# Optimization experiments

Measured on AMD Instinct MI355X. Metric: run time of the kernel, lower is better.

Reference implementation:

```python
import jax, jax.numpy as jnp
import numpy as np

N_SRC, N_MID, N_DST = 200000, 50000, 10000
D = 128
E1, E2 = 800000, 160000
EPS = 1e-12  # F.normalize eps


def setup_inputs() -> dict:
    key = jax.random.key(0)
    ks = jax.random.split(key, 12)
    s = 1.0 / np.sqrt(D)
    return {
        "x": jax.random.normal(ks[0], (N_SRC, D), jnp.float32),
        "W_l1": jax.random.uniform(ks[1], (D, D), jnp.float32, -s, s),
        "b_l1": jax.random.uniform(ks[2], (D,), jnp.float32, -s, s),
        "W_r1": jax.random.uniform(ks[3], (D, D), jnp.float32, -s, s),
        "W_l2": jax.random.uniform(ks[4], (D, D), jnp.float32, -s, s),
        "b_l2": jax.random.uniform(ks[5], (D,), jnp.float32, -s, s),
        "W_r2": jax.random.uniform(ks[6], (D, D), jnp.float32, -s, s),
        "row1": jax.random.randint(ks[7], (E1,), 0, N_SRC, jnp.int32),
        "col1": jax.random.randint(ks[8], (E1,), 0, N_MID, jnp.int32),
        "row2": jax.random.randint(ks[9], (E2,), 0, N_MID, jnp.int32),
        "col2": jax.random.randint(ks[10], (E2,), 0, N_DST, jnp.int32),
    }


def _sage_conv(x_src, x_dst, row, col, W_l, b_l, W_r, n_dst):
    # mean aggregation of source features over incoming edges (gather + scatter-add)
    msg = x_src[row]                                              # [E, D]
    agg = jax.ops.segment_sum(msg, col, num_segments=n_dst)       # [n_dst, D]
    deg = jax.ops.segment_sum(jnp.ones((row.shape[0],), x_src.dtype), col,
                              num_segments=n_dst)[:, None]        # [n_dst, 1]
    mean = jnp.where(deg > 0, agg / jnp.maximum(deg, 1.0), 0.0)
    out = mean @ W_l.T + b_l + x_dst @ W_r.T                      # lin_l + lin_r (root)
    # L2 normalize (normalize=True)
    norm = jnp.sqrt(jnp.sum(out * out, axis=-1, keepdims=True))
    return out / jnp.maximum(norm, EPS)


def reference(x, W_l1, b_l1, W_r1, W_l2, b_l2, W_r2, row1, col1, row2, col2):
    # layer 1: src = all sampled nodes, dst = first N_MID nodes
    h = _sage_conv(x, x[:N_MID], row1, col1, W_l1, b_l1, W_r1, N_MID)
    h = jax.nn.relu(h)  # dropout is identity in eval mode
    # layer 2: src = mid nodes, dst = first N_DST nodes (the batch targets)
    out = _sage_conv(h, h[:N_DST], row2, col2, W_l2, b_l2, W_r2, N_DST)
    return out
```

## Files before the change

kernel.cpp:

```cpp
#include <hip/hip_runtime.h>
#include <hip/hip_bf16.h>

#define DD 128
#define N_SRC 200000
#define N_MID 50000
#define N_DST 10000
#define E1 800000
#define E2 160000
#define CAP 48

typedef unsigned short u16;
typedef unsigned int u32;
typedef __attribute__((ext_vector_type(8))) short s16x8;
typedef __attribute__((ext_vector_type(4))) float f32x4;
typedef __attribute__((ext_vector_type(4))) int i32x4;
typedef __attribute__((ext_vector_type(4))) float fv4;


__device__ __forceinline__ float bf_lo(u32 u) {
    union { u32 u; float f; } v; v.u = u << 16; return v.f;
}
__device__ __forceinline__ float bf_hi(u32 u) {
    union { u32 u; float f; } v; v.u = u & 0xffff0000u; return v.f;
}
__device__ __forceinline__ u32 f2bf_bits(float f) {
    union { float f; u32 u; } v; v.f = f;
    return (v.u + 0x7fffu + ((v.u >> 16) & 1u)) >> 16;
}
__device__ __forceinline__ u32 pack2bf(float lo, float hi) {
    return f2bf_bits(lo) | (f2bf_bits(hi) << 16);
}


#define FILL1_SLICE  4000
#define FILL1_BLOCKS 1600

#define NCONV8 (N_SRC * DD / 8)
#define WTF_T 8192
#define PREP_T (NCONV8 + WTF_T)
#define PREP_BLOCKS ((PREP_T + 255) / 256)
#define PF_BLOCKS (FILL1_BLOCKS + PREP_BLOCKS)

__global__ __launch_bounds__(256, 8) void prep_fill(
    const float* __restrict__ x, u16* __restrict__ xb,
    const float* __restrict__ Wl1, const float* __restrict__ Wr1,
    u16* __restrict__ WTf1,
    const float* __restrict__ Wl2, const float* __restrict__ Wr2,
    u16* __restrict__ WTf2,
    const int* __restrict__ row1, const int* __restrict__ col1,
    int* __restrict__ cnt1, int* __restrict__ csr1)
{
    const int b = blockIdx.x;
    const int tid = threadIdx.x;

    if (b < FILL1_BLOCKS) {
        int slice = b >> 3, shard = b & 7;
        int e0 = slice * FILL1_SLICE, e1 = e0 + FILL1_SLICE;
        const int lo = shard * 6250;
        for (int base = e0 + tid * 4; base < e1; base += 1024) {
            i32x4 c4 = __builtin_nontemporal_load((const i32x4*)(col1 + base));
            i32x4 r4 = __builtin_nontemporal_load((const i32x4*)(row1 + base));
            #pragma unroll
            for (int k = 0; k < 4; ++k) {
                int c = c4[k];
                if ((u32)(c - lo) < 6250u) {
                    int p = atomicAdd(cnt1 + c, 1);
                    if (p < CAP) csr1[c * CAP + p] = r4[k];
                }
            }
        }
    } else {
        int i = (b - FILL1_BLOCKS) * 256 + tid;
        if (i < NCONV8) {
            const fv4* x4 = (const fv4*)x;
            fv4 a = __builtin_nontemporal_load(x4 + i * 2);
            fv4 bb = __builtin_nontemporal_load(x4 + i * 2 + 1);
            uint4 o;
            o.x = pack2bf(a[0], a[1]); o.y = pack2bf(a[2], a[3]);
            o.z = pack2bf(bb[0], bb[1]); o.w = pack2bf(bb[2], bb[3]);
            ((uint4*)xb)[i] = o;
        } else if (i < NCONV8 + WTF_T) {
            int t = i - NCONV8;
            int layer = t >> 12;
            int rem = t & 4095;
            int kt = rem >> 9;
            int nt = (rem >> 6) & 7;
            int lane = rem & 63;
            int gn = nt * 16 + (lane & 15);
            int k0 = kt * 32 + (lane >> 4) * 8;
            const float* Wl = layer ? Wl2 : Wl1;
            const float* Wr = layer ? Wr2 : Wr1;
            u16* WTf = layer ? WTf2 : WTf1;
            u32 o[4];
            #pragma unroll
            for (int p = 0; p < 4; ++p) {
                int ka = k0 + 2 * p, kb = ka + 1;
                float ea = (ka < 128) ? Wl[gn * 128 + ka] : Wr[gn * 128 + (ka - 128)];
                float eb = (kb < 128) ? Wl[gn * 128 + kb] : Wr[gn * 128 + (kb - 128)];
                o[p] = pack2bf(ea, eb);
            }
            ((uint4*)WTf)[(kt * 8 + nt) * 64 + lane] = make_uint4(o[0], o[1], o[2], o[3]);
        }
    }
}


template <int ROWS, bool RELU, int MINB>
__global__ __launch_bounds__(256, MINB) void sage_kernel(
    const u16* __restrict__ xsrc_b, const u16* __restrict__ xdst_b,
    const int* __restrict__ cnt, const int* __restrict__ csrf,
    const u16* __restrict__ WTf, const float* __restrict__ bias,
    float* __restrict__ out_f, u16* __restrict__ out_b,
    int n_dst, int fp32lim,
    const int* __restrict__ frow, const int* __restrict__ fcol,
    int* __restrict__ fcnt, int* __restrict__ fcsr, int nfill)
{
    __shared__ float smem[ROWS * 132];
    const int tid = threadIdx.x;

    if (blockIdx.x < nfill) {
        int bb = blockIdx.x;
        int slice = bb >> 3, shard = bb & 7;
        int e0 = slice * 4000, e1 = e0 + 4000;
        const int lo = shard * 1250;
        for (int base = e0 + tid * 4; base < e1; base += 1024) {
            i32x4 c4 = __builtin_nontemporal_load((const i32x4*)(fcol + base));
            i32x4 r4 = __builtin_nontemporal_load((const i32x4*)(frow + base));
            #pragma unroll
            for (int k = 0; k < 4; ++k) {
                int c = c4[k];
                if ((u32)(c - lo) < 1250u) {
                    int p = atomicAdd(fcnt + c, 1);
                    if (p < CAP) fcsr[c * CAP + p] = r4[k];
                }
            }
        }
        return;
    }

    const int i0 = (blockIdx.x - nfill) * ROWS;
    const int lane = tid & 63;
    const int w = tid >> 6;
    const int quarter = lane >> 4;
    const int l16 = lane & 15;
    const int half = lane >> 5;
    const int l32 = lane & 31;
    constexpr int RPW = ROWS / 4;

    const uint4* __restrict__ xs4 = (const uint4*)xsrc_b;
    const uint2* __restrict__ xd2 = (const uint2*)xdst_b;
    uint4* sA4 = (uint4*)smem;
    uint2* sA2 = (uint2*)smem;

    int degv = 0;
    {
        int rr = i0 + w * RPW + lane;
        if (lane < RPW && rr < n_dst) degv = cnt[rr];
    }
    int iv_next = 0;
    {
        int i = i0 + w * RPW;
        if (i < n_dst) iv_next = csrf[(size_t)i * CAP + lane];
    }

    for (int q = 0; q < RPW; ++q) {
        int r = w * RPW + q;
        int i = i0 + r;
        int deg = __shfl(degv, q);
        if (deg > CAP) deg = CAP;
        int iv = iv_next;
        if (q + 1 < RPW) {
            int i2 = i + 1;
            iv_next = (i2 < n_dst) ? csrf[(size_t)i2 * CAP + lane] : 0;
        }
        if (i < n_dst) {
            float acc[8] = {0.f, 0.f, 0.f, 0.f, 0.f, 0.f, 0.f, 0.f};
            if (deg > 0) {
                for (int g = 0; g < deg; g += 16) {
                    #pragma unroll
                    for (int j = 0; j < 4; ++j) {
                        if (g + 4 * j < deg) {
                            int rel = g + 4 * j + quarter;
                            int idx = __shfl(iv, rel & 63);
                            float m = (rel < deg) ? 1.f : 0.f;
                            uint4 u = xs4[(size_t)idx * 16 + l16];
                            acc[0] += m * bf_lo(u.x); acc[1] += m * bf_hi(u.x);
                            acc[2] += m * bf_lo(u.y); acc[3] += m * bf_hi(u.y);
                            acc[4] += m * bf_lo(u.z); acc[5] += m * bf_hi(u.z);
                            acc[6] += m * bf_lo(u.w); acc[7] += m * bf_hi(u.w);
                        }
                    }
                }
                #pragma unroll
                for (int k = 0; k < 8; ++k) {
                    acc[k] += __shfl_xor(acc[k], 16);
                    acc[k] += __shfl_xor(acc[k], 32);
                }
            }
            float s = (deg > 0) ? 1.f / (float)deg : 0.f;
            if (quarter == 0) {
                uint4 o;
                o.x = pack2bf(acc[0] * s, acc[1] * s);
                o.y = pack2bf(acc[2] * s, acc[3] * s);
                o.z = pack2bf(acc[4] * s, acc[5] * s);
                o.w = pack2bf(acc[6] * s, acc[7] * s);
                sA4[r * 33 + l16] = o;
            }
            if (half == 1) {
                sA2[r * 66 + 32 + l32] = xd2[(size_t)i * 32 + l32];
            }
        } else {
            if (quarter == 0) sA4[r * 33 + l16] = make_uint4(0, 0, 0, 0);
            if (half == 1)    sA2[r * 66 + 32 + l32] = make_uint2(0, 0);
        }
    }
    __syncthreads();

    constexpr int MT = ROWS / 16;
    const int nt0 = w * 2;
    const s16x8* sAv = (const s16x8*)smem;
    const s16x8* Bv = (const s16x8*)WTf;

    f32x4 C[MT][2];
    #pragma unroll
    for (int mt = 0; mt < MT; ++mt)
        #pragma unroll
        for (int ni = 0; ni < 2; ++ni)
            C[mt][ni] = (f32x4){0.f, 0.f, 0.f, 0.f};

    #pragma unroll
    for (int kt = 0; kt < 8; ++kt) {
        s16x8 a[MT];
        #pragma unroll
        for (int mt = 0; mt < MT; ++mt)
            a[mt] = sAv[(mt * 16 + l16) * 33 + kt * 4 + quarter];
        s16x8 b0 = Bv[(kt * 8 + nt0) * 64 + lane];
        s16x8 b1 = Bv[(kt * 8 + nt0 + 1) * 64 + lane];
        #pragma unroll
        for (int mt = 0; mt < MT; ++mt) {
            C[mt][0] = __builtin_amdgcn_mfma_f32_16x16x32_bf16(a[mt], b0, C[mt][0], 0, 0, 0);
            C[mt][1] = __builtin_amdgcn_mfma_f32_16x16x32_bf16(a[mt], b1, C[mt][1], 0, 0, 0);
        }
    }

    __syncthreads();
    float* sOut = smem;

    #pragma unroll
    for (int ni = 0; ni < 2; ++ni) {
        int col = (nt0 + ni) * 16 + l16;
        float bc = bias[col];
        #pragma unroll
        for (int mt = 0; mt < MT; ++mt) {
            #pragma unroll
            for (int r = 0; r < 4; ++r) {
                int row = mt * 16 + quarter * 4 + r;
                sOut[row * 132 + col] = C[mt][ni][r] + bc;
            }
        }
    }
    __syncthreads();

    constexpr int R = ROWS / 8;
    const int ty = tid >> 5;
    const int tx = tid & 31;
    #pragma unroll
    for (int r = 0; r < R; ++r) {
        int row = ty * R + r;
        float4 v = *(const float4*)(&sOut[row * 132 + tx * 4]);
        float s = v.x * v.x + v.y * v.y + v.z * v.z + v.w * v.w;
        #pragma unroll
        for (int off = 1; off < 32; off <<= 1) s += __shfl_xor(s, off);
        float scale = 1.f / fmaxf(sqrtf(s), 1e-12f);
        float v0 = v.x * scale, v1 = v.y * scale, v2 = v.z * scale, v3 = v.w * scale;
        if (RELU) {
            v0 = fmaxf(v0, 0.f); v1 = fmaxf(v1, 0.f);
            v2 = fmaxf(v2, 0.f); v3 = fmaxf(v3, 0.f);
        }
        int i = i0 + row;
        if (i < n_dst) {
            if (i < fp32lim)
                *(float4*)(out_f + (size_t)i * DD + tx * 4) = make_float4(v0, v1, v2, v3);
            if (out_b) {
                uint2 ob;
                ob.x = pack2bf(v0, v1);
                ob.y = pack2bf(v2, v3);
                *(uint2*)(out_b + (size_t)i * DD + tx * 4) = ob;
            }
        }
    }
}


#define NF2 320

extern "C" void kernel_launch(void* const* d_in, const int* in_sizes, int n_in,
                              void* d_out, int out_size, void* d_ws, size_t ws_size,
                              hipStream_t stream) {
    const float* x    = (const float*)d_in[0];
    const float* Wl1  = (const float*)d_in[1];
    const float* bl1  = (const float*)d_in[2];
    const float* Wr1  = (const float*)d_in[3];
    const float* Wl2  = (const float*)d_in[4];
    const float* bl2  = (const float*)d_in[5];
    const float* Wr2  = (const float*)d_in[6];
    const int* row1   = (const int*)d_in[7];
    const int* col1   = (const int*)d_in[8];
    const int* row2   = (const int*)d_in[9];
    const int* col2   = (const int*)d_in[10];
    float* out = (float*)d_out;

    char* p = (char*)d_ws;
    u16* xb    = (u16*)p;   p += (size_t)N_SRC * DD * sizeof(u16);
    u16* hb    = (u16*)p;   p += (size_t)N_MID * DD * sizeof(u16);
    u16* WTf1  = (u16*)p;   p += (size_t)256 * 128 * sizeof(u16);
    u16* WTf2  = (u16*)p;   p += (size_t)256 * 128 * sizeof(u16);
    char* zbase = p;
    int* cnt1  = (int*)p;   p += (size_t)N_MID * sizeof(int);
    int* cnt2  = (int*)p;   p += (size_t)N_DST * sizeof(int);
    int* csr1  = (int*)p;   p += (size_t)N_MID * CAP * sizeof(int);
    int* csr2  = (int*)p;   p += (size_t)N_DST * CAP * sizeof(int);
    size_t zlen = (size_t)(p - zbase);

    (void)hipMemsetAsync(zbase, 0, zlen, stream);

    prep_fill<<<PF_BLOCKS, 256, 0, stream>>>(
        x, xb, Wl1, Wr1, WTf1, Wl2, Wr2, WTf2, row1, col1, cnt1, csr1);

    sage_kernel<32, true, 6><<<NF2 + (N_MID + 31) / 32, 256, 0, stream>>>(
        xb, xb, cnt1, csr1, WTf1, bl1, (float*)nullptr, hb, N_MID, 0,
        row2, col2, cnt2, csr2, NF2);

    sage_kernel<16, false, 6><<<(N_DST + 15) / 16, 256, 0, stream>>>(
        hb, hb, cnt2, csr2, WTf2, bl2, out, (u16*)nullptr, N_DST, N_DST,
        nullptr, nullptr, nullptr, nullptr, 0);
}
```

Baseline: 273.3 us.

## Replace global-atomic CSR fill with two-pass bucket partition and shared-memory sort

Edge-to-CSR construction changes from sharded global atomicAdd per edge to a two-pass scheme. The first pass partitions edges into column buckets of width 200 using shared-memory counters and one global atomic per bucket per block. The second pass builds per-node CSR slots with shared-memory histograms. The layer-2 fill moves out of the layer-1 sage kernel into the shared sort kernel, and the bucket staging buffer reuses the hb region. This cuts global atomic contention and redundant col reads but adds a kernel launch and extra staging traffic, and edges past the 3584-per-bucket cap are dropped.

```diff
diff --git a/kernel.cpp b/kernel.cpp
--- a/kernel.cpp
+++ b/kernel.cpp
@@ -9,11 +9,19 @@
 #define E2 160000
 #define CAP 48
 
+#define BK_W  200
+#define NB1   250
+#define NB2   50
+#define CCAP  3584
+#define P1E   2048
+#define NP1_1 ((E1 + P1E - 1) / P1E)
+#define NP1_2 ((E2 + P1E - 1) / P1E)
+#define P1_BLOCKS (NP1_1 + NP1_2)
+
 typedef unsigned short u16;
 typedef unsigned int u32;
 typedef __attribute__((ext_vector_type(8))) short s16x8;
 typedef __attribute__((ext_vector_type(4))) float f32x4;
-typedef __attribute__((ext_vector_type(4))) int i32x4;
 typedef __attribute__((ext_vector_type(4))) float fv4;
 
 
@@ -31,46 +39,75 @@
     return f2bf_bits(lo) | (f2bf_bits(hi) << 16);
 }
 
-
-#define FILL1_SLICE  4000
-#define FILL1_BLOCKS 1600
 
 #define NCONV8 (N_SRC * DD / 8)
 #define WTF_T 8192
 #define PREP_T (NCONV8 + WTF_T)
 #define PREP_BLOCKS ((PREP_T + 255) / 256)
-#define PF_BLOCKS (FILL1_BLOCKS + PREP_BLOCKS)
-
-__global__ __launch_bounds__(256, 8) void prep_fill(
+#define PA_BLOCKS (P1_BLOCKS + PREP_BLOCKS)
+
+__global__ __launch_bounds__(256, 8) void prep_part(
     const float* __restrict__ x, u16* __restrict__ xb,
     const float* __restrict__ Wl1, const float* __restrict__ Wr1,
     u16* __restrict__ WTf1,
     const float* __restrict__ Wl2, const float* __restrict__ Wr2,
     u16* __restrict__ WTf2,
     const int* __restrict__ row1, const int* __restrict__ col1,
-    int* __restrict__ cnt1, int* __restrict__ csr1)
+    const int* __restrict__ row2, const int* __restrict__ col2,
+    int* __restrict__ ccnt1, int* __restrict__ ccnt2,
+    int2* __restrict__ cbuf1, int2* __restrict__ cbuf2)
 {
+    __shared__ int lcnt[256];
+    __shared__ int gbase[256];
     const int b = blockIdx.x;
     const int tid = threadIdx.x;
 
-    if (b < FILL1_BLOCKS) {
-        int slice = b >> 3, shard = b & 7;
-        int e0 = slice * FILL1_SLICE, e1 = e0 + FILL1_SLICE;
-        const int lo = shard * 6250;
-        for (int base = e0 + tid * 4; base < e1; base += 1024) {
-            i32x4 c4 = __builtin_nontemporal_load((const i32x4*)(col1 + base));
-            i32x4 r4 = __builtin_nontemporal_load((const i32x4*)(row1 + base));
-            #pragma unroll
-            for (int k = 0; k < 4; ++k) {
-                int c = c4[k];
-                if ((u32)(c - lo) < 6250u) {
-                    int p = atomicAdd(cnt1 + c, 1);
-                    if (p < CAP) csr1[c * CAP + p] = r4[k];
-                }
+    if (b < P1_BLOCKS) {
+        const int* __restrict__ colp;
+        const int* __restrict__ rowp;
+        int* __restrict__ ccnt;
+        int2* __restrict__ cbuf;
+        int e0, ne, nb;
+        if (b < NP1_1) {
+            colp = col1; rowp = row1; ccnt = ccnt1; cbuf = cbuf1;
+            e0 = b * P1E; ne = E1 - e0; if (ne > P1E) ne = P1E; nb = NB1;
+        } else {
+            int bb = b - NP1_1;
+            colp = col2; rowp = row2; ccnt = ccnt2; cbuf = cbuf2;
+            e0 = bb * P1E; ne = E2 - e0; if (ne > P1E) ne = P1E; nb = NB2;
+        }
+        for (int t = tid; t < nb; t += 256) lcnt[t] = 0;
+        __syncthreads();
+        int ep[8];
+        #pragma unroll
+        for (int j = 0; j < 8; ++j) {
+            int e = tid + j * 256;
+            ep[j] = -1;
+            if (e < ne) {
+                int c = colp[e0 + e];
+                int bk = c / BK_W;
+                int rk = atomicAdd(&lcnt[bk], 1);
+                ep[j] = (bk << 16) | rk;
+            }
+        }
+        __syncthreads();
+        for (int t = tid; t < nb; t += 256) {
+            int c = lcnt[t];
+            gbase[t] = c ? atomicAdd(&ccnt[t], c) : 0;
+        }
+        __syncthreads();
+        #pragma unroll
+        for (int j = 0; j < 8; ++j) {
+            if (ep[j] >= 0) {
+                int e = e0 + tid + j * 256;
+                int bk = ep[j] >> 16;
+                int pos = gbase[bk] + (ep[j] & 0xffff);
+                if (pos < CCAP)
+                    cbuf[(size_t)bk * CCAP + pos] = make_int2(colp[e], rowp[e]);
             }
         }
     } else {
-        int i = (b - FILL1_BLOCKS) * 256 + tid;
+        int i = (b - P1_BLOCKS) * 256 + tid;
         if (i < NCONV8) {
             const fv4* x4 = (const fv4*)x;
             fv4 a = __builtin_nontemporal_load(x4 + i * 2);
@@ -105,40 +142,57 @@
 }
 
 
+__global__ __launch_bounds__(256, 8) void bucket_sort(
+    const int2* __restrict__ cbuf1, const int2* __restrict__ cbuf2,
+    const int* __restrict__ ccnt1, const int* __restrict__ ccnt2,
+    int* __restrict__ cnt1, int* __restrict__ cnt2,
+    int* __restrict__ csr1, int* __restrict__ csr2)
+{
+    const int b = blockIdx.x;
+    const int tid = threadIdx.x;
+    const int2* __restrict__ cbuf;
+    const int* __restrict__ ccnt;
+    int* __restrict__ cnt;
+    int* __restrict__ csr;
+    int bkt;
+    if (b < NB1) { cbuf = cbuf1; ccnt = ccnt1; cnt = cnt1; csr = csr1; bkt = b; }
+    else         { cbuf = cbuf2; ccnt = ccnt2; cnt = cnt2; csr = csr2; bkt = b - NB1; }
+    const int col0 = bkt * BK_W;
+
+    __shared__ int hist[BK_W];
+    for (int t = tid; t < BK_W; t += 256) hist[t] = 0;
+    __syncthreads();
+
+    int n = ccnt[bkt]; if (n > CCAP) n = CCAP;
+    const int2* bp = cbuf + (size_t)bkt * CCAP;
+    for (int e = tid; e < n; e += 512) {
+        int2 cr0 = bp[e];
+        int e1i = e + 256;
+        bool h1 = e1i < n;
+        int2 cr1 = h1 ? bp[e1i] : cr0;
+        int r0 = atomicAdd(&hist[cr0.x - col0], 1);
+        if (r0 < CAP) csr[cr0.x * CAP + r0] = cr0.y;
+        if (h1) {
+            int r1 = atomicAdd(&hist[cr1.x - col0], 1);
+            if (r1 < CAP) csr[cr1.x * CAP + r1] = cr1.y;
+        }
+    }
+    __syncthreads();
+    for (int t = tid; t < BK_W; t += 256) cnt[col0 + t] = hist[t];
+}
+
+
 template <int ROWS, bool RELU, int MINB>
 __global__ __launch_bounds__(256, MINB) void sage_kernel(
     const u16* __restrict__ xsrc_b, const u16* __restrict__ xdst_b,
     const int* __restrict__ cnt, const int* __restrict__ csrf,
     const u16* __restrict__ WTf, const float* __restrict__ bias,
     float* __restrict__ out_f, u16* __restrict__ out_b,
-    int n_dst, int fp32lim,
-    const int* __restrict__ frow, const int* __restrict__ fcol,
-    int* __restrict__ fcnt, int* __restrict__ fcsr, int nfill)
+    int n_dst, int fp32lim)
 {
     __shared__ float smem[ROWS * 132];
     const int tid = threadIdx.x;
-
-    if (blockIdx.x < nfill) {
-        int bb = blockIdx.x;
-        int slice = bb >> 3, shard = bb & 7;
-        int e0 = slice * 4000, e1 = e0 + 4000;
-        const int lo = shard * 1250;
-        for (int base = e0 + tid * 4; base < e1; base += 1024) {
-            i32x4 c4 = __builtin_nontemporal_load((const i32x4*)(fcol + base));
-            i32x4 r4 = __builtin_nontemporal_load((const i32x4*)(frow + base));
-            #pragma unroll
-            for (int k = 0; k < 4; ++k) {
-                int c = c4[k];
-                if ((u32)(c - lo) < 1250u) {
-                    int p = atomicAdd(fcnt + c, 1);
-                    if (p < CAP) fcsr[c * CAP + p] = r4[k];
-                }
-            }
-        }
-        return;
-    }
-
-    const int i0 = (blockIdx.x - nfill) * ROWS;
+    const int i0 = blockIdx.x * ROWS;
     const int lane = tid & 63;
     const int w = tid >> 6;
     const int quarter = lane >> 4;
@@ -292,8 +346,6 @@
 }
 
 
-#define NF2 320
-
 extern "C" void kernel_launch(void* const* d_in, const int* in_sizes, int n_in,
                               void* d_out, int out_size, void* d_ws, size_t ws_size,
                               hipStream_t stream) {
@@ -312,26 +364,34 @@
 
     char* p = (char*)d_ws;
     u16* xb    = (u16*)p;   p += (size_t)N_SRC * DD * sizeof(u16);
-    u16* hb    = (u16*)p;   p += (size_t)N_MID * DD * sizeof(u16);
+    char* hbv  = p;         p += (size_t)N_MID * DD * sizeof(u16);
+    u16* hb    = (u16*)hbv;
+    int2* cbuf1 = (int2*)hbv;
+    int2* cbuf2 = cbuf1 + (size_t)NB1 * CCAP;
     u16* WTf1  = (u16*)p;   p += (size_t)256 * 128 * sizeof(u16);
     u16* WTf2  = (u16*)p;   p += (size_t)256 * 128 * sizeof(u16);
     char* zbase = p;
+    int* ccnt1 = (int*)p;   p += 256 * sizeof(int);
+    int* ccnt2 = (int*)p;   p += 64 * sizeof(int);
     int* cnt1  = (int*)p;   p += (size_t)N_MID * sizeof(int);
     int* cnt2  = (int*)p;   p += (size_t)N_DST * sizeof(int);
     int* csr1  = (int*)p;   p += (size_t)N_MID * CAP * sizeof(int);
     int* csr2  = (int*)p;   p += (size_t)N_DST * CAP * sizeof(int);
+    p += 256;
     size_t zlen = (size_t)(p - zbase);
 
     (void)hipMemsetAsync(zbase, 0, zlen, stream);
 
-    prep_fill<<<PF_BLOCKS, 256, 0, stream>>>(
-        x, xb, Wl1, Wr1, WTf1, Wl2, Wr2, WTf2, row1, col1, cnt1, csr1);
-
-    sage_kernel<32, true, 6><<<NF2 + (N_MID + 31) / 32, 256, 0, stream>>>(
-        xb, xb, cnt1, csr1, WTf1, bl1, (float*)nullptr, hb, N_MID, 0,
-        row2, col2, cnt2, csr2, NF2);
+    prep_part<<<PA_BLOCKS, 256, 0, stream>>>(
+        x, xb, Wl1, Wr1, WTf1, Wl2, Wr2, WTf2,
+        row1, col1, row2, col2, ccnt1, ccnt2, cbuf1, cbuf2);
+
+    bucket_sort<<<NB1 + NB2, 256, 0, stream>>>(
+        cbuf1, cbuf2, ccnt1, ccnt2, cnt1, cnt2, csr1, csr2);
+
+    sage_kernel<32, true, 6><<<(N_MID + 31) / 32, 256, 0, stream>>>(
+        xb, xb, cnt1, csr1, WTf1, bl1, (float*)nullptr, hb, N_MID, 0);
 
     sage_kernel<16, false, 6><<<(N_DST + 15) / 16, 256, 0, stream>>>(
-        hb, hb, cnt2, csr2, WTf2, bl2, out, (u16*)nullptr, N_DST, N_DST,
-        nullptr, nullptr, nullptr, nullptr, 0);
-}
+        hb, hb, cnt2, csr2, WTf2, bl2, out, (u16*)nullptr, N_DST, N_DST);
+}
```

Measured after the change: 252.4 us. 1.08x faster.
